# Performance work log

Hardware: AMD Instinct MI355X
Metric: run time of the kernel (lower is better)

The kernel has to match this reference:

```python
import jax, jax.numpy as jnp
import numpy as np

D_MODEL = 2048
NUM_HEADS = 16
D_K = D_MODEL // NUM_HEADS
THETA = 10000.0
MAX_SEQ_LEN = 2048
B, S = 2, 2048


def setup_inputs() -> dict:
    key = jax.random.key(0)
    ks = jax.random.split(key, 5)
    x = jax.random.normal(ks[0], (B, S, D_MODEL), dtype=jnp.float32)
    token_positions = jnp.tile(jnp.arange(S, dtype=jnp.int64 if jax.config.jax_enable_x64 else jnp.int32), (B, 1))
    wq = jax.random.normal(ks[1], (D_MODEL, D_MODEL), dtype=jnp.float32)
    wk = jax.random.normal(ks[2], (D_MODEL, D_MODEL), dtype=jnp.float32)
    wv = jax.random.normal(ks[3], (D_MODEL, D_MODEL), dtype=jnp.float32)
    wo = jax.random.normal(ks[4], (D_MODEL, D_MODEL), dtype=jnp.float32)
    return {"x": x, "token_positions": token_positions, "wq": wq, "wk": wk, "wv": wv, "wo": wo}


def _rope_tables():
    # inv freqs: exp(arange(0,d_k,2) * (-log(theta)/d_k))  -> [d_k/2]
    inv_freq = jnp.exp(jnp.arange(0, D_K, 2, dtype=jnp.float32) * (-np.log(THETA) / D_K))
    m = jnp.arange(MAX_SEQ_LEN, dtype=jnp.float32)[:, None]  # [L,1]
    ang = m * inv_freq[None, :]                               # [L, d_k/2]
    return jnp.cos(ang), jnp.sin(ang)


def _apply_rope(x, token_positions, cos_tab, sin_tab):
    # x: [B, H, S, d_k]; token_positions: [B, S]
    cos = cos_tab[token_positions][:, None, :, :]  # [B,1,S,d_k/2]
    sin = sin_tab[token_positions][:, None, :, :]
    xe = x[..., 0::2]
    xo = x[..., 1::2]
    re = xe * cos - xo * sin
    ro = xo * cos + xe * sin
    out = jnp.stack([re, ro], axis=-1).reshape(x.shape)
    return out


def reference(x, token_positions, wq, wk, wv, wo):
    b, s, _ = x.shape
    cos_tab, sin_tab = _rope_tables()

    def split_heads(t):  # [B,S,D] -> [B,H,S,d_k]
        return t.reshape(b, s, NUM_HEADS, D_K).transpose(0, 2, 1, 3)

    q = _apply_rope(split_heads(x @ wq), token_positions, cos_tab, sin_tab)
    k = _apply_rope(split_heads(x @ wk), token_positions, cos_tab, sin_tab)
    v = split_heads(x @ wv)

    scores = jnp.einsum("bhqd,bhkd->bhqk", q, k) / jnp.sqrt(jnp.float32(D_K))
    causal = jnp.tril(jnp.ones((s, s), dtype=bool))
    scores = jnp.where(causal[None, None], scores, jnp.float32(-1e9))
    attn = jax.nn.softmax(scores, axis=-1)
    out = jnp.einsum("bhqk,bhkd->bhqd", attn, v)
    out = out.transpose(0, 2, 1, 3).reshape(b, s, D_MODEL)
    return out @ wo
```

## Files before the change

### kernel.cpp

```cpp
#include <hip/hip_runtime.h>
#include <hip/hip_bf16.h>
#include <cstdio>

namespace {

constexpr int kSeq = 2048;
constexpr int kDModel = 2048;
constexpr int kHeads = 16;
constexpr int kDk = 128;
constexpr int kBatch = 2;
constexpr int kM = kBatch * kSeq;
constexpr float kQScale = 0.08838834764831845f;

typedef __bf16 bf16_t;
typedef __bf16 bf16x8 __attribute__((ext_vector_type(8)));
typedef __bf16 bf16x4 __attribute__((ext_vector_type(4)));
typedef float f32x4 __attribute__((ext_vector_type(4)));
typedef short s16x4 __attribute__((ext_vector_type(4)));

__device__ __forceinline__ f32x4 mfma32(bf16x8 a, bf16x8 b, f32x4 c) {
  return __builtin_amdgcn_mfma_f32_16x16x32_bf16(a, b, c, 0, 0, 0);
}

#if __has_builtin(__builtin_amdgcn_mfma_f32_16x16x16_bf16)
__device__ __forceinline__ f32x4 mfma16(bf16x4 a, bf16x4 b, f32x4 c) {
  return __builtin_amdgcn_mfma_f32_16x16x16_bf16(a, b, c, 0, 0, 0);
}
#else
__device__ __forceinline__ f32x4 mfma16(bf16x4 a, bf16x4 b, f32x4 c) {
  union U { bf16x4 b; s16x4 s; } ua, ub;
  ua.b = a; ub.b = b;
  return __builtin_amdgcn_mfma_f32_16x16x16bf16_1k(ua.s, ub.s, c, 0, 0, 0);
}
#endif

using gas_void = const __attribute__((address_space(1))) void;
using las_void = __attribute__((address_space(3))) void;

__device__ __forceinline__ void gload_lds16(const bf16_t* g, bf16_t* l) {
  __builtin_amdgcn_global_load_lds((gas_void*)g, (las_void*)l, 16, 0, 0);
}

__global__ void k_rope_table(float* __restrict__ cost, float* __restrict__ sint) {
  const int p = blockIdx.x;
  const int i = threadIdx.x;
  const double inv = exp(-(double)(2 * i) * 9.210340371976184 / 128.0);
  const double ang = (double)p * inv;
  cost[p * 64 + i] = (float)cos(ang);
  sint[p * 64 + i] = (float)sin(ang);
}

__global__ void k_split_x(const float* __restrict__ x, bf16_t* __restrict__ xh,
                          bf16_t* __restrict__ xl, int n) {
  const int idx = (blockIdx.x * blockDim.x + threadIdx.x) * 4;
  if (idx >= n) return;
  const float4 v = *(const float4*)(x + idx);
  const float vv[4] = {v.x, v.y, v.z, v.w};
  bf16x4 hv, lv;
#pragma unroll
  for (int j = 0; j < 4; ++j) {
    const bf16_t h = (bf16_t)vv[j];
    hv[j] = h;
    lv[j] = (bf16_t)(vv[j] - (float)h);
  }
  *(bf16x4*)(xh + idx) = hv;
  *(bf16x4*)(xl + idx) = lv;
}

__global__ void k_transpose_w(const float* __restrict__ w, bf16_t* __restrict__ wth,
                              bf16_t* __restrict__ wtl) {
  __shared__ float tile[32][33];
  const int bx = blockIdx.x * 32;
  const int by = blockIdx.y * 32;
  const int tx = threadIdx.x, ty = threadIdx.y;
#pragma unroll
  for (int i = 0; i < 32; i += 8)
    tile[ty + i][tx] = w[(size_t)(by + ty + i) * kDModel + bx + tx];
  __syncthreads();
#pragma unroll
  for (int i = 0; i < 32; i += 8) {
    const float v = tile[tx][ty + i];
    const size_t o = (size_t)(bx + ty + i) * kDModel + by + tx;
    const bf16_t h = (bf16_t)v;
    wth[o] = h;
    if (wtl) wtl[o] = (bf16_t)(v - (float)h);
  }
}

template <int TERMS, int EPI>
__global__ __launch_bounds__(256) void k_gemm(
    const bf16_t* __restrict__ Ah, const bf16_t* __restrict__ Al,
    const bf16_t* __restrict__ Bh, const bf16_t* __restrict__ Bl,
    void* __restrict__ O0, void* __restrict__ O1,
    const int* __restrict__ tokpos, const float* __restrict__ cost,
    const float* __restrict__ sint, float scale, int M, int N, int K) {
  __shared__ __align__(16) bf16_t sAh[128 * 32];
  __shared__ __align__(16) bf16_t sBh[128 * 32];
  __shared__ __align__(16) bf16_t sAl[TERMS == 3 ? 128 * 32 : 8];
  __shared__ __align__(16) bf16_t sBl[TERMS == 3 ? 128 * 32 : 8];

  const int tid = threadIdx.x;
  const int wid = tid >> 6;
  const int lane = tid & 63;
  const int lo = lane & 15, hi = lane >> 4;
  const int wr = wid >> 1, wc = wid & 1;
  const int flat = blockIdx.x + blockIdx.y * gridDim.x;
  const int wgid = (flat & 7) * ((gridDim.x * gridDim.y) >> 3) + (flat >> 3);
  const int m0 = (wgid / gridDim.x) * 128, n0 = (wgid % gridDim.x) * 128;

  f32x4 acc[4][4];
  const f32x4 z = {0.f, 0.f, 0.f, 0.f};
#pragma unroll
  for (int i = 0; i < 4; ++i)
#pragma unroll
    for (int j = 0; j < 4; ++j) acc[i][j] = z;

  const int rr = wid * 16 + (lane >> 2);
  const int kk = (lane & 3) * 8;

  for (int k0 = 0; k0 < K; k0 += 32) {
    __syncthreads();
    {
      const bf16_t* gA = Ah + (size_t)(m0 + rr) * K + k0 + kk;
      gload_lds16(gA, sAh + wid * 512);
      gload_lds16(gA + (size_t)64 * K, sAh + 2048 + wid * 512);
      const bf16_t* gB = Bh + (size_t)(n0 + rr) * K + k0 + kk;
      gload_lds16(gB, sBh + wid * 512);
      gload_lds16(gB + (size_t)64 * K, sBh + 2048 + wid * 512);
      if constexpr (TERMS == 3) {
        const bf16_t* gAl = Al + (size_t)(m0 + rr) * K + k0 + kk;
        gload_lds16(gAl, sAl + wid * 512);
        gload_lds16(gAl + (size_t)64 * K, sAl + 2048 + wid * 512);
        const bf16_t* gBl = Bl + (size_t)(n0 + rr) * K + k0 + kk;
        gload_lds16(gBl, sBl + wid * 512);
        gload_lds16(gBl + (size_t)64 * K, sBl + 2048 + wid * 512);
      }
    }
    __syncthreads();
    bf16x8 fah[4], fbh[4];
#pragma unroll
    for (int mi = 0; mi < 4; ++mi)
      fah[mi] = *(const bf16x8*)(sAh + (wr * 64 + mi * 16 + lo) * 32 + 8 * hi);
#pragma unroll
    for (int ni = 0; ni < 4; ++ni)
      fbh[ni] = *(const bf16x8*)(sBh + (wc * 64 + ni * 16 + lo) * 32 + 8 * hi);
    if constexpr (TERMS == 3) {
      bf16x8 fal[4], fbl[4];
#pragma unroll
      for (int mi = 0; mi < 4; ++mi)
        fal[mi] = *(const bf16x8*)(sAl + (wr * 64 + mi * 16 + lo) * 32 + 8 * hi);
#pragma unroll
      for (int ni = 0; ni < 4; ++ni)
        fbl[ni] = *(const bf16x8*)(sBl + (wc * 64 + ni * 16 + lo) * 32 + 8 * hi);
#pragma unroll
      for (int mi = 0; mi < 4; ++mi)
#pragma unroll
        for (int ni = 0; ni < 4; ++ni) {
          acc[mi][ni] = mfma32(fah[mi], fbh[ni], acc[mi][ni]);
          acc[mi][ni] = mfma32(fah[mi], fbl[ni], acc[mi][ni]);
          acc[mi][ni] = mfma32(fal[mi], fbh[ni], acc[mi][ni]);
        }
    } else {
#pragma unroll
      for (int mi = 0; mi < 4; ++mi)
#pragma unroll
        for (int ni = 0; ni < 4; ++ni)
          acc[mi][ni] = mfma32(fah[mi], fbh[ni], acc[mi][ni]);
    }
  }

  if constexpr (EPI == 0) {
    float* C = (float*)O0;
#pragma unroll
    for (int mi = 0; mi < 4; ++mi)
#pragma unroll
      for (int ni = 0; ni < 4; ++ni)
#pragma unroll
        for (int r = 0; r < 4; ++r) {
          const int row = m0 + wr * 64 + mi * 16 + hi * 4 + r;
          const int col = n0 + wc * 64 + ni * 16 + lo;
          C[(size_t)row * N + col] = acc[mi][ni][r];
        }
  } else if constexpr (EPI == 1) {
    bf16_t* Xh = (bf16_t*)O0;
    bf16_t* Xl = (bf16_t*)O1;
    const int is64 = (tokpos[1] == 0) ? 1 : 0;
#pragma unroll
    for (int mi = 0; mi < 4; ++mi) {
#pragma unroll
      for (int r = 0; r < 4; ++r) {
        const int row = m0 + wr * 64 + mi * 16 + hi * 4 + r;
        const int pos = is64 ? tokpos[2 * row] : tokpos[row];
#pragma unroll
        for (int ni = 0; ni < 4; ++ni) {
          const int col = n0 + wc * 64 + ni * 16 + lo;
          const float v = acc[mi][ni][r] * scale;
          const float pv = __shfl_xor(v, 1);
          const int ip = (col & 127) >> 1;
          const float c = cost[pos * 64 + ip];
          const float sn = sint[pos * 64 + ip];
          const float sgn = (lo & 1) ? sn : -sn;
          const float rv = v * c + pv * sgn;
          const bf16_t hb = (bf16_t)rv;
          const size_t o = (size_t)row * N + col;
          Xh[o] = hb;
          Xl[o] = (bf16_t)(rv - (float)hb);
        }
      }
    }
  } else {
    bf16_t* VT = (bf16_t*)O0;
#pragma unroll
    for (int mi = 0; mi < 4; ++mi)
#pragma unroll
      for (int ni = 0; ni < 4; ++ni) {
        const int col = n0 + wc * 64 + ni * 16 + lo;
        const int h = col >> 7, d = col & 127;
        const int rowb = m0 + wr * 64 + mi * 16 + hi * 4;
        const int b = rowb >> 11, s = rowb & (kSeq - 1);
        bf16x4 ov;
#pragma unroll
        for (int r = 0; r < 4; ++r) ov[r] = (bf16_t)acc[mi][ni][r];
        *(bf16x4*)(VT + ((size_t)((b * kHeads + h) * kDk + d)) * kSeq + s) = ov;
      }
  }
}

__global__ __launch_bounds__(512, 2) void k_attn4(
    const bf16_t* __restrict__ Qh, const bf16_t* __restrict__ Ql,
    const bf16_t* __restrict__ Kh, const bf16_t* __restrict__ Kl,
    const bf16_t* __restrict__ VT, bf16_t* __restrict__ Ob) {
  __shared__ __align__(16) bf16_t sK[2][2][64 * 128];
  __shared__ __align__(16) bf16_t sV[2][128 * 64];

  const int tid = threadIdx.x;
  const int wid = tid >> 6, lane = tid & 63;
  const int lo = lane & 15, hi = lane >> 4;
  const int flat = blockIdx.x;
  const int j = flat >> 3;
  const int bh = (flat & 7) * 4 + (j & 3);
  const int p = j >> 2;
  const int b = bh >> 4, h = bh & 15;
  const int qiW = (wid < 4) ? (15 - p) : p;
  const int qw = qiW * 128 + (wid & 3) * 32;
  const int nkv = 2 * (15 - p) + 2;

  bf16x8 qhf[4][2], qlf[4][2];
  {
    const size_t qbase =
        (size_t)(b * kSeq + qw + lo) * kDModel + h * kDk + hi * 8;
#pragma unroll
    for (int qt = 0; qt < 2; ++qt)
#pragma unroll
      for (int ks = 0; ks < 4; ++ks) {
        const size_t o = qbase + (size_t)qt * 16 * kDModel + ks * 32;
        qhf[ks][qt] = *(const bf16x8*)(Qh + o);
        qlf[ks][qt] = *(const bf16x8*)(Ql + o);
      }
  }

  const int rK0 = wid * 8 + (lane >> 4);
  const int gK0 = ((lane & 15) ^ (rK0 & 15)) * 8;
  const int gK1 = ((lane & 15) ^ ((rK0 + 4) & 15)) * 8;
  const bf16_t* pKh0 = Kh + (size_t)(b * kSeq + rK0) * kDModel + h * kDk + gK0;
  const bf16_t* pKh1 = Kh + (size_t)(b * kSeq + rK0 + 4) * kDModel + h * kDk + gK1;
  const bf16_t* pKl0 = Kl + (pKh0 - Kh);
  const bf16_t* pKl1 = Kl + (pKh1 - Kh);
  const int dV0 = wid * 16 + (lane >> 3);
  const int gV0 = ((lane & 7) ^ (dV0 & 7)) * 8;
  const int gV1 = ((lane & 7) ^ ((dV0 + 8) & 7)) * 8;
  const bf16_t* pV0 = VT + (size_t)(bh * kDk + dV0) * kSeq + gV0;
  const bf16_t* pV1 = VT + (size_t)(bh * kDk + dV0 + 8) * kSeq + gV1;
  const int ldsK = (wid * 8) * 128;
  const int ldsV = (wid * 16) * 64;

  f32x4 of[8][2];
  const f32x4 z = {0.f, 0.f, 0.f, 0.f};
#pragma unroll
  for (int di = 0; di < 8; ++di) {
    of[di][0] = z;
    of[di][1] = z;
  }
  float m[2] = {-3e38f, -3e38f};
  float l[2] = {0.f, 0.f};

  auto STAGE = [&](int buf, int t) {
    const size_t ko = (size_t)t * 64 * kDModel;
    const size_t vo = (size_t)t * 64;
    bf16_t* dk = sK[buf][0] + ldsK;
    bf16_t* dl = sK[buf][1] + ldsK;
    gload_lds16(pKh0 + ko, dk);
    gload_lds16(pKh1 + ko, dk + 512);
    gload_lds16(pKl0 + ko, dl);
    gload_lds16(pKl1 + ko, dl + 512);
    bf16_t* dv = sV[buf] + ldsV;
    gload_lds16(pV0 + vo, dv);
    gload_lds16(pV1 + vo, dv + 512);
  };

  STAGE(0, 0);
  __syncthreads();

  for (int t = 0; t < nkv; ++t) {
    const int kv0 = t * 64;
    if (t + 1 < nkv) STAGE((t + 1) & 1, t + 1);

    if (kv0 <= qw + 31) {
      const bf16_t* bKh = sK[t & 1][0];
      const bf16_t* bKl = sK[t & 1][1];
      const bf16_t* bV = sV[t & 1];
      const bool maskedw = (kv0 + 63 > qw);

      f32x4 st[4][2];
#pragma unroll
      for (int kt = 0; kt < 4; ++kt) {
        st[kt][0] = z;
        st[kt][1] = z;
      }
#pragma unroll
      for (int kt = 0; kt < 4; ++kt) {
#pragma unroll
        for (int ks = 0; ks < 4; ++ks) {
          const int krow = kt * 16 + lo;
          const int ka = krow * 128 + (((ks * 4 + hi) ^ (krow & 15)) * 8);
          const bf16x8 kh8 = *(const bf16x8*)(bKh + ka);
          const bf16x8 kl8 = *(const bf16x8*)(bKl + ka);
#pragma unroll
          for (int qt = 0; qt < 2; ++qt) {
            st[kt][qt] = mfma32(kh8, qhf[ks][qt], st[kt][qt]);
            st[kt][qt] = mfma32(kh8, qlf[ks][qt], st[kt][qt]);
            st[kt][qt] = mfma32(kl8, qhf[ks][qt], st[kt][qt]);
          }
        }
      }

      bf16x4 pb[4][2];
#pragma unroll
      for (int qt = 0; qt < 2; ++qt) {
        const int q = qw + qt * 16 + lo;
        float mt = -3e38f;
#pragma unroll
        for (int kt = 0; kt < 4; ++kt)
#pragma unroll
          for (int r = 0; r < 4; ++r) {
            float s = st[kt][qt][r];
            if (maskedw && (kv0 + kt * 16 + hi * 4 + r > q)) s = -1e30f;
            st[kt][qt][r] = s;
            mt = fmaxf(mt, s);
          }
        mt = fmaxf(mt, __shfl_xor(mt, 16));
        mt = fmaxf(mt, __shfl_xor(mt, 32));
        if (!__all(mt <= m[qt] + 8.f)) {
          const float mnew = fmaxf(m[qt], mt);
          const float corr = __expf(m[qt] - mnew);
          l[qt] *= corr;
#pragma unroll
          for (int di = 0; di < 8; ++di) of[di][qt] = of[di][qt] * corr;
          m[qt] = mnew;
        }
        float rs = 0.f;
#pragma unroll
        for (int kt = 0; kt < 4; ++kt) {
          bf16x4 pv;
#pragma unroll
          for (int r = 0; r < 4; ++r) {
            const float pp = __expf(st[kt][qt][r] - m[qt]);
            rs += pp;
            pv[r] = (bf16_t)pp;
          }
          pb[kt][qt] = pv;
        }
        rs += __shfl_xor(rs, 16);
        rs += __shfl_xor(rs, 32);
        l[qt] += rs;
      }

#pragma unroll
      for (int di = 0; di < 8; ++di) {
        const int d = di * 16 + lo;
#pragma unroll
        for (int kt = 0; kt < 4; ++kt) {
          const int va =
              d * 64 + (((kt * 2 + (hi >> 1)) ^ (d & 7)) * 8) + (hi & 1) * 4;
          const bf16x4 vf = *(const bf16x4*)(bV + va);
          of[di][0] = mfma16(vf, pb[kt][0], of[di][0]);
          of[di][1] = mfma16(vf, pb[kt][1], of[di][1]);
        }
      }
    }
    __syncthreads();
  }

#pragma unroll
  for (int qt = 0; qt < 2; ++qt) {
    const float linv = 1.f / l[qt];
    const size_t ob =
        (size_t)(b * kSeq + qw + qt * 16 + lo) * kDModel + h * kDk + hi * 4;
#pragma unroll
    for (int di = 0; di < 8; ++di) {
      bf16x4 ov;
#pragma unroll
      for (int r = 0; r < 4; ++r) ov[r] = (bf16_t)(of[di][qt][r] * linv);
      *(bf16x4*)(Ob + ob + di * 16) = ov;
    }
  }
}

}

extern "C" void kernel_launch(void* const* d_in, const int* in_sizes, int n_in,
                              void* d_out, int out_size, void* d_ws, size_t ws_size,
                              hipStream_t stream) {
  (void)in_sizes; (void)n_in; (void)out_size;
  const float* x = (const float*)d_in[0];
  const int* tokpos = (const int*)d_in[1];
  const float* wq = (const float*)d_in[2];
  const float* wk = (const float*)d_in[3];
  const float* wv = (const float*)d_in[4];
  const float* wo = (const float*)d_in[5];
  float* out = (float*)d_out;

  char* p = (char*)d_ws;
  auto take = [&](size_t bytes) { char* q = p; p += bytes; return q; };
  float* cost = (float*)take((size_t)kSeq * 64 * sizeof(float));
  float* sint = (float*)take((size_t)kSeq * 64 * sizeof(float));
  const size_t mat = (size_t)kM * kDModel * sizeof(bf16_t);
  const size_t wmat = (size_t)kDModel * kDModel * sizeof(bf16_t);
  bf16_t* xh = (bf16_t*)take(mat);
  bf16_t* xl = (bf16_t*)take(mat);
  bf16_t* wqth = (bf16_t*)take(wmat);
  bf16_t* wqtl = (bf16_t*)take(wmat);
  bf16_t* wkth = (bf16_t*)take(wmat);
  bf16_t* wktl = (bf16_t*)take(wmat);
  bf16_t* wvt = (bf16_t*)take(wmat);
  bf16_t* wot = (bf16_t*)take(wmat);
  bf16_t* qh = (bf16_t*)take(mat);
  bf16_t* ql = (bf16_t*)take(mat);
  bf16_t* kh = (bf16_t*)take(mat);
  bf16_t* kl = (bf16_t*)take(mat);
  bf16_t* vt = (bf16_t*)take(mat);
  bf16_t* ob = (bf16_t*)take(mat);
  if ((size_t)(p - (char*)d_ws) > ws_size) {
    fprintf(stderr, "MHA: workspace too small: need %zu have %zu\n",
            (size_t)(p - (char*)d_ws), ws_size);
    return;
  }

  k_rope_table<<<dim3(kSeq), dim3(64), 0, stream>>>(cost, sint);
  k_split_x<<<dim3((kM * kDModel) / (256 * 4)), dim3(256), 0, stream>>>(
      x, xh, xl, kM * kDModel);
  {
    dim3 tb(32, 8), tg(kDModel / 32, kDModel / 32);
    k_transpose_w<<<tg, tb, 0, stream>>>(wq, wqth, wqtl);
    k_transpose_w<<<tg, tb, 0, stream>>>(wk, wkth, wktl);
    k_transpose_w<<<tg, tb, 0, stream>>>(wv, wvt, nullptr);
    k_transpose_w<<<tg, tb, 0, stream>>>(wo, wot, nullptr);
  }
  const dim3 gg(kDModel / 128, kM / 128);
  k_gemm<3, 1><<<gg, 256, 0, stream>>>(xh, xl, wqth, wqtl, qh, ql, tokpos, cost,
                                       sint, kQScale, kM, kDModel, kDModel);
  k_gemm<3, 1><<<gg, 256, 0, stream>>>(xh, xl, wkth, wktl, kh, kl, tokpos, cost,
                                       sint, 1.0f, kM, kDModel, kDModel);
  k_gemm<1, 2><<<gg, 256, 0, stream>>>(xh, nullptr, wvt, nullptr, vt, nullptr,
                                       nullptr, nullptr, nullptr, 1.0f, kM,
                                       kDModel, kDModel);
  k_attn4<<<dim3(256), dim3(512), 0, stream>>>(qh, ql, kh, kl, vt, ob);
  k_gemm<1, 0><<<gg, 256, 0, stream>>>(ob, nullptr, wot, nullptr, out, nullptr,
                                       nullptr, nullptr, nullptr, 1.0f, kM,
                                       kDModel, kDModel);
}
```

Measured before the change: 467.4 us.

## Replace GEMM with 256x128 triple-buffered swizzled kernel and fuse Q/K projections

Replaces the 128x128 single-buffered GEMM with a 512-thread kernel using 256x128 tiles, a 64-wide K step and XOR-swizzled LDS. A three-slot LDS ring prefetches two tiles ahead, with split barriers and raised wave priority around the MFMA blocks. The three-term bf16 split is expressed as a single K loop over concatenated (hi·hi, hi·lo, lo·hi) tiles. Q and K projections share one launch over a concatenated transposed weight, with the epilogue choosing the output buffers and scale. This is meant to hide global load latency and raise MFMA utilization, but it uses roughly 147KB of LDS per block, which limits occupancy.

```diff
diff --git a/kernel.cpp b/kernel.cpp
--- a/kernel.cpp
+++ b/kernel.cpp
@@ -88,25 +88,72 @@
 }
 
 template <int TERMS, int EPI>
-__global__ __launch_bounds__(256) void k_gemm(
+__global__ __launch_bounds__(512) void k_gemm8(
     const bf16_t* __restrict__ Ah, const bf16_t* __restrict__ Al,
     const bf16_t* __restrict__ Bh, const bf16_t* __restrict__ Bl,
-    void* __restrict__ O0, void* __restrict__ O1,
-    const int* __restrict__ tokpos, const float* __restrict__ cost,
-    const float* __restrict__ sint, float scale, int M, int N, int K) {
-  __shared__ __align__(16) bf16_t sAh[128 * 32];
-  __shared__ __align__(16) bf16_t sBh[128 * 32];
-  __shared__ __align__(16) bf16_t sAl[TERMS == 3 ? 128 * 32 : 8];
-  __shared__ __align__(16) bf16_t sBl[TERMS == 3 ? 128 * 32 : 8];
+    void* __restrict__ O0, void* __restrict__ O1, void* __restrict__ O2,
+    void* __restrict__ O3, const int* __restrict__ tokpos,
+    const float* __restrict__ cost, const float* __restrict__ sint, int NT,
+    int ntk) {
+  __shared__ __align__(16) bf16_t sA[3][256 * 64];
+  __shared__ __align__(16) bf16_t sB[3][128 * 64];
 
   const int tid = threadIdx.x;
-  const int wid = tid >> 6;
-  const int lane = tid & 63;
+  const int wid = tid >> 6, lane = tid & 63;
   const int lo = lane & 15, hi = lane >> 4;
-  const int wr = wid >> 1, wc = wid & 1;
-  const int flat = blockIdx.x + blockIdx.y * gridDim.x;
-  const int wgid = (flat & 7) * ((gridDim.x * gridDim.y) >> 3) + (flat >> 3);
-  const int m0 = (wgid / gridDim.x) * 128, n0 = (wgid % gridDim.x) * 128;
+  const int wrr = wid >> 1, wcc = wid & 1;
+  const int x7 = lo & 7;
+
+  const int bid = blockIdx.x;
+  const int wgid = (bid & 7) * (gridDim.x >> 3) + (bid >> 3);
+  const int mt = wgid / NT, nt = wgid % NT;
+  const int m0 = mt * 256, n0 = nt * 128;
+
+  const int rB = tid >> 3;
+  const int ch8 = ((tid & 7) ^ (rB & 7)) * 8;
+  size_t offA[4], offB[2];
+#pragma unroll
+  for (int u = 0; u < 2; ++u)
+#pragma unroll
+    for (int i = 0; i < 2; ++i)
+      offA[u * 2 + i] = (size_t)(m0 + u * 128 + i * 64 + rB) * 2048 + ch8;
+#pragma unroll
+  for (int i = 0; i < 2; ++i)
+    offB[i] = (size_t)(n0 + i * 64 + rB) * 2048 + ch8;
+  const int ldsOff = wid * 512;
+
+  auto STAGE_A = [&](int slot, int t) {
+    const bf16_t* base;
+    if constexpr (TERMS == 3)
+      base = (t < 64 ? Ah : Al) + (t & 31) * 64;
+    else
+      base = Ah + t * 64;
+    bf16_t* d = sA[slot] + ldsOff;
+#pragma unroll
+    for (int ui = 0; ui < 4; ++ui) gload_lds16(base + offA[ui], d + ui * 4096);
+  };
+  auto STAGE_B = [&](int slot, int t) {
+    const bf16_t* base;
+    if constexpr (TERMS == 3)
+      base = (((t >> 5) == 1) ? Bl : Bh) + (t & 31) * 64;
+    else
+      base = Bh + t * 64;
+    bf16_t* d = sB[slot] + ldsOff;
+#pragma unroll
+    for (int i = 0; i < 2; ++i) gload_lds16(base + offB[i], d + i * 4096);
+  };
+
+  int aoff[4][2], boff[4][2];
+#pragma unroll
+  for (int mi = 0; mi < 4; ++mi)
+#pragma unroll
+    for (int ks = 0; ks < 2; ++ks)
+      aoff[mi][ks] = (wrr * 64 + mi * 16 + lo) * 64 + (((ks * 4 + hi) ^ x7) * 8);
+#pragma unroll
+  for (int ni = 0; ni < 4; ++ni)
+#pragma unroll
+    for (int ks = 0; ks < 2; ++ks)
+      boff[ni][ks] = (wcc * 64 + ni * 16 + lo) * 64 + (((ks * 4 + hi) ^ x7) * 8);
 
   f32x4 acc[4][4];
   const f32x4 z = {0.f, 0.f, 0.f, 0.f};
@@ -115,58 +162,72 @@
 #pragma unroll
     for (int j = 0; j < 4; ++j) acc[i][j] = z;
 
-  const int rr = wid * 16 + (lane >> 2);
-  const int kk = (lane & 3) * 8;
-
-  for (int k0 = 0; k0 < K; k0 += 32) {
-    __syncthreads();
-    {
-      const bf16_t* gA = Ah + (size_t)(m0 + rr) * K + k0 + kk;
-      gload_lds16(gA, sAh + wid * 512);
-      gload_lds16(gA + (size_t)64 * K, sAh + 2048 + wid * 512);
-      const bf16_t* gB = Bh + (size_t)(n0 + rr) * K + k0 + kk;
-      gload_lds16(gB, sBh + wid * 512);
-      gload_lds16(gB + (size_t)64 * K, sBh + 2048 + wid * 512);
-      if constexpr (TERMS == 3) {
-        const bf16_t* gAl = Al + (size_t)(m0 + rr) * K + k0 + kk;
-        gload_lds16(gAl, sAl + wid * 512);
-        gload_lds16(gAl + (size_t)64 * K, sAl + 2048 + wid * 512);
-        const bf16_t* gBl = Bl + (size_t)(n0 + rr) * K + k0 + kk;
-        gload_lds16(gBl, sBl + wid * 512);
-        gload_lds16(gBl + (size_t)64 * K, sBl + 2048 + wid * 512);
-      }
-    }
-    __syncthreads();
-    bf16x8 fah[4], fbh[4];
-#pragma unroll
-    for (int mi = 0; mi < 4; ++mi)
-      fah[mi] = *(const bf16x8*)(sAh + (wr * 64 + mi * 16 + lo) * 32 + 8 * hi);
+  STAGE_A(0, 0);
+  STAGE_B(0, 0);
+  STAGE_A(1, 1);
+  STAGE_B(1, 1);
+  asm volatile("s_waitcnt vmcnt(6)" ::: "memory");
+  __builtin_amdgcn_s_barrier();
+  asm volatile("" ::: "memory");
+
+  int s0 = 0;
+  for (int t = 0; t < ntk; ++t) {
+    const bf16_t* sa = sA[s0];
+    const bf16_t* sb = sB[s0];
+    int s2 = s0 + 2;
+    if (s2 >= 3) s2 -= 3;
+    const bool pf = (t + 2 < ntk);
+
+    bf16x8 af[2][2], bfr[4][2];
+#pragma unroll
+    for (int mi = 0; mi < 2; ++mi)
+#pragma unroll
+      for (int ks = 0; ks < 2; ++ks)
+        af[mi][ks] = *(const bf16x8*)(sa + aoff[mi][ks]);
 #pragma unroll
     for (int ni = 0; ni < 4; ++ni)
-      fbh[ni] = *(const bf16x8*)(sBh + (wc * 64 + ni * 16 + lo) * 32 + 8 * hi);
-    if constexpr (TERMS == 3) {
-      bf16x8 fal[4], fbl[4];
-#pragma unroll
-      for (int mi = 0; mi < 4; ++mi)
-        fal[mi] = *(const bf16x8*)(sAl + (wr * 64 + mi * 16 + lo) * 32 + 8 * hi);
-#pragma unroll
-      for (int ni = 0; ni < 4; ++ni)
-        fbl[ni] = *(const bf16x8*)(sBl + (wc * 64 + ni * 16 + lo) * 32 + 8 * hi);
-#pragma unroll
-      for (int mi = 0; mi < 4; ++mi)
-#pragma unroll
-        for (int ni = 0; ni < 4; ++ni) {
-          acc[mi][ni] = mfma32(fah[mi], fbh[ni], acc[mi][ni]);
-          acc[mi][ni] = mfma32(fah[mi], fbl[ni], acc[mi][ni]);
-          acc[mi][ni] = mfma32(fal[mi], fbh[ni], acc[mi][ni]);
-        }
-    } else {
-#pragma unroll
-      for (int mi = 0; mi < 4; ++mi)
-#pragma unroll
-        for (int ni = 0; ni < 4; ++ni)
-          acc[mi][ni] = mfma32(fah[mi], fbh[ni], acc[mi][ni]);
-    }
+#pragma unroll
+      for (int ks = 0; ks < 2; ++ks)
+        bfr[ni][ks] = *(const bf16x8*)(sb + boff[ni][ks]);
+    if (pf) STAGE_A(s2, t + 2);
+    asm volatile("" ::: "memory");
+    __builtin_amdgcn_s_barrier();
+    asm volatile("" ::: "memory");
+    __builtin_amdgcn_s_setprio(1);
+#pragma unroll
+    for (int ni = 0; ni < 4; ++ni)
+#pragma unroll
+      for (int mi = 0; mi < 2; ++mi)
+#pragma unroll
+        for (int ks = 0; ks < 2; ++ks)
+          acc[mi][ni] = mfma32(af[mi][ks], bfr[ni][ks], acc[mi][ni]);
+    __builtin_amdgcn_s_setprio(0);
+
+    bf16x8 ag[2][2];
+#pragma unroll
+    for (int mi = 0; mi < 2; ++mi)
+#pragma unroll
+      for (int ks = 0; ks < 2; ++ks)
+        ag[mi][ks] = *(const bf16x8*)(sa + aoff[2 + mi][ks]);
+    if (pf) STAGE_B(s2, t + 2);
+    if (pf)
+      asm volatile("s_waitcnt vmcnt(6)" ::: "memory");
+    else
+      asm volatile("s_waitcnt vmcnt(0)" ::: "memory");
+    __builtin_amdgcn_s_barrier();
+    asm volatile("" ::: "memory");
+    __builtin_amdgcn_s_setprio(1);
+#pragma unroll
+    for (int ni = 0; ni < 4; ++ni)
+#pragma unroll
+      for (int mi = 0; mi < 2; ++mi)
+#pragma unroll
+        for (int ks = 0; ks < 2; ++ks)
+          acc[2 + mi][ni] = mfma32(ag[mi][ks], bfr[ni][ks], acc[2 + mi][ni]);
+    __builtin_amdgcn_s_setprio(0);
+
+    s0 += 1;
+    if (s0 >= 3) s0 = 0;
   }
 
   if constexpr (EPI == 0) {
@@ -177,23 +238,25 @@
       for (int ni = 0; ni < 4; ++ni)
 #pragma unroll
         for (int r = 0; r < 4; ++r) {
-          const int row = m0 + wr * 64 + mi * 16 + hi * 4 + r;
-          const int col = n0 + wc * 64 + ni * 16 + lo;
-          C[(size_t)row * N + col] = acc[mi][ni][r];
+          const int row = m0 + wrr * 64 + mi * 16 + hi * 4 + r;
+          const int col = n0 + wcc * 64 + ni * 16 + lo;
+          C[(size_t)row * 2048 + col] = acc[mi][ni][r];
         }
   } else if constexpr (EPI == 1) {
-    bf16_t* Xh = (bf16_t*)O0;
-    bf16_t* Xl = (bf16_t*)O1;
+    const int qk = n0 >> 11;
+    bf16_t* Xh = (bf16_t*)(qk ? O2 : O0);
+    bf16_t* Xl = (bf16_t*)(qk ? O3 : O1);
+    const float scale = qk ? 1.0f : kQScale;
     const int is64 = (tokpos[1] == 0) ? 1 : 0;
 #pragma unroll
     for (int mi = 0; mi < 4; ++mi) {
 #pragma unroll
       for (int r = 0; r < 4; ++r) {
-        const int row = m0 + wr * 64 + mi * 16 + hi * 4 + r;
+        const int row = m0 + wrr * 64 + mi * 16 + hi * 4 + r;
         const int pos = is64 ? tokpos[2 * row] : tokpos[row];
 #pragma unroll
         for (int ni = 0; ni < 4; ++ni) {
-          const int col = n0 + wc * 64 + ni * 16 + lo;
+          const int col = n0 + wcc * 64 + ni * 16 + lo;
           const float v = acc[mi][ni][r] * scale;
           const float pv = __shfl_xor(v, 1);
           const int ip = (col & 127) >> 1;
@@ -202,7 +265,7 @@
           const float sgn = (lo & 1) ? sn : -sn;
           const float rv = v * c + pv * sgn;
           const bf16_t hb = (bf16_t)rv;
-          const size_t o = (size_t)row * N + col;
+          const size_t o = (size_t)row * 2048 + (col & 2047);
           Xh[o] = hb;
           Xl[o] = (bf16_t)(rv - (float)hb);
         }
@@ -214,9 +277,9 @@
     for (int mi = 0; mi < 4; ++mi)
 #pragma unroll
       for (int ni = 0; ni < 4; ++ni) {
-        const int col = n0 + wc * 64 + ni * 16 + lo;
+        const int col = n0 + wcc * 64 + ni * 16 + lo;
         const int h = col >> 7, d = col & 127;
-        const int rowb = m0 + wr * 64 + mi * 16 + hi * 4;
+        const int rowb = m0 + wrr * 64 + mi * 16 + hi * 4;
         const int b = rowb >> 11, s = rowb & (kSeq - 1);
         bf16x4 ov;
 #pragma unroll
@@ -428,10 +491,8 @@
   const size_t wmat = (size_t)kDModel * kDModel * sizeof(bf16_t);
   bf16_t* xh = (bf16_t*)take(mat);
   bf16_t* xl = (bf16_t*)take(mat);
-  bf16_t* wqth = (bf16_t*)take(wmat);
-  bf16_t* wqtl = (bf16_t*)take(wmat);
-  bf16_t* wkth = (bf16_t*)take(wmat);
-  bf16_t* wktl = (bf16_t*)take(wmat);
+  bf16_t* wqkth = (bf16_t*)take(2 * wmat);
+  bf16_t* wqktl = (bf16_t*)take(2 * wmat);
   bf16_t* wvt = (bf16_t*)take(wmat);
   bf16_t* wot = (bf16_t*)take(wmat);
   bf16_t* qh = (bf16_t*)take(mat);
@@ -451,21 +512,19 @@
       x, xh, xl, kM * kDModel);
   {
     dim3 tb(32, 8), tg(kDModel / 32, kDModel / 32);
-    k_transpose_w<<<tg, tb, 0, stream>>>(wq, wqth, wqtl);
-    k_transpose_w<<<tg, tb, 0, stream>>>(wk, wkth, wktl);
+    k_transpose_w<<<tg, tb, 0, stream>>>(wq, wqkth, wqktl);
+    k_transpose_w<<<tg, tb, 0, stream>>>(wk, wqkth + (size_t)2048 * 2048,
+                                         wqktl + (size_t)2048 * 2048);
     k_transpose_w<<<tg, tb, 0, stream>>>(wv, wvt, nullptr);
     k_transpose_w<<<tg, tb, 0, stream>>>(wo, wot, nullptr);
   }
-  const dim3 gg(kDModel / 128, kM / 128);
-  k_gemm<3, 1><<<gg, 256, 0, stream>>>(xh, xl, wqth, wqtl, qh, ql, tokpos, cost,
-                                       sint, kQScale, kM, kDModel, kDModel);
-  k_gemm<3, 1><<<gg, 256, 0, stream>>>(xh, xl, wkth, wktl, kh, kl, tokpos, cost,
-                                       sint, 1.0f, kM, kDModel, kDModel);
-  k_gemm<1, 2><<<gg, 256, 0, stream>>>(xh, nullptr, wvt, nullptr, vt, nullptr,
-                                       nullptr, nullptr, nullptr, 1.0f, kM,
-                                       kDModel, kDModel);
+  k_gemm8<3, 1><<<dim3(512), dim3(512), 0, stream>>>(
+      xh, xl, wqkth, wqktl, qh, ql, kh, kl, tokpos, cost, sint, 32, 96);
+  k_gemm8<1, 2><<<dim3(256), dim3(512), 0, stream>>>(
+      xh, nullptr, wvt, nullptr, vt, nullptr, nullptr, nullptr, nullptr,
+      nullptr, nullptr, 16, 32);
   k_attn4<<<dim3(256), dim3(512), 0, stream>>>(qh, ql, kh, kl, vt, ob);
-  k_gemm<1, 0><<<gg, 256, 0, stream>>>(ob, nullptr, wot, nullptr, out, nullptr,
-                                       nullptr, nullptr, nullptr, 1.0f, kM,
-                                       kDModel, kDModel);
-}
+  k_gemm8<1, 0><<<dim3(256), dim3(512), 0, stream>>>(
+      ob, nullptr, wot, nullptr, out, nullptr, nullptr, nullptr, nullptr,
+      nullptr, nullptr, 16, 32);
+}
```

New measurement: 437.5 us. 6.4% less time.
